# Optimization experiments

Hardware: AMD Instinct MI355X
Metric: run time of the kernel (lower is better)

## Reference

```python
import jax, jax.numpy as jnp
import numpy as np

DROPOUT_P = 0.1
DROPOUT_KEY = 42  # fixed key so the reference is deterministic


def setup_inputs() -> dict:
    key = jax.random.key(0)
    kx, kw = jax.random.split(key)
    B, N, D = 8, 2048, 1024
    x = jax.random.normal(kx, (B, N, D), dtype=jnp.float32)
    # xavier_uniform_ on [D, D]: U(-a, a), a = sqrt(6 / (D + D))
    a = np.sqrt(6.0 / (D + D)).astype(np.float32)
    weight = jax.random.uniform(kw, (D, D), dtype=jnp.float32, minval=-a, maxval=a)
    return {"x": x, "weight": weight}


def reference(x, weight):
    # bilinear scores: (x @ W) @ x^T  -> [B, N, N]
    scores = jnp.einsum("bnd,de,bme->bnm", x, weight, x)
    attn = jax.nn.softmax(scores, axis=-1)
    # dropout (train-mode, inverted scaling), deterministic key
    keep = jax.random.bernoulli(jax.random.key(DROPOUT_KEY), 1.0 - DROPOUT_P, attn.shape)
    attn = jnp.where(keep, attn / (1.0 - DROPOUT_P), 0.0)
    return jnp.einsum("bnm,bmd->bnd", attn, x)
```

## Files before the change

kernel.cpp:

```cpp
#include <hip/hip_runtime.h>
#include <hip/hip_fp16.h>
#include <stdint.h>

typedef __attribute__((ext_vector_type(8))) _Float16 f16x8;
typedef __attribute__((ext_vector_type(4))) float f32x4;
typedef __attribute__((ext_vector_type(8))) short s16x8;

#define MFMA_F16(a, b, c) __builtin_amdgcn_mfma_f32_16x16x32_f16((a), (b), (c), 0, 0, 0)
#define MFMA_BF16(a, b, c) __builtin_amdgcn_mfma_f32_16x16x32_bf16((a), (b), (c), 0, 0, 0)

__device__ __forceinline__ uint32_t pack_hi2(float f0, float f1, float& r0, float& r1) {
  uint32_t b0 = __float_as_uint(f0), b1 = __float_as_uint(f1);
  r0 = f0 - __uint_as_float(b0 & 0xFFFF0000u);
  r1 = f1 - __uint_as_float(b1 & 0xFFFF0000u);
  return (b1 & 0xFFFF0000u) | (b0 >> 16);
}
__device__ __forceinline__ uint32_t pack_lo2(float r0, float r1) {
  return (__float_as_uint(r1) & 0xFFFF0000u) | (__float_as_uint(r0) >> 16);
}
__device__ __forceinline__ uint32_t f16rn(float f) {
  return (uint32_t)__half_as_ushort(__float2half_rn(f));
}
__device__ __forceinline__ float f16tof(uint32_t h) {
  return __half2float(__ushort_as_half((unsigned short)h));
}

__device__ __forceinline__ uint2 threefry2x32_42(uint32_t x0, uint32_t x1) {
  const uint32_t ks0 = 0u, ks1 = 42u, ks2 = 0x1BD11BDAu ^ 42u;
  x0 += ks0; x1 += ks1;
#define TF_R(rot) { x0 += x1; x1 = ((x1 << rot) | (x1 >> (32 - rot))); x1 ^= x0; }
  TF_R(13) TF_R(15) TF_R(26) TF_R(6)   x0 += ks1; x1 += ks2 + 1u;
  TF_R(17) TF_R(29) TF_R(16) TF_R(24)  x0 += ks2; x1 += ks0 + 2u;
  TF_R(13) TF_R(15) TF_R(26) TF_R(6)   x0 += ks0; x1 += ks1 + 3u;
  TF_R(17) TF_R(29) TF_R(16) TF_R(24)  x0 += ks1; x1 += ks2 + 4u;
  TF_R(13) TF_R(15) TF_R(26) TF_R(6)   x0 += ks2; x1 += ks0 + 5u;
#undef TF_R
  return make_uint2(x0, x1);
}
__device__ __forceinline__ bool keep_bit(uint32_t j) {
  uint2 tf = threefry2x32_42(0u, j);
  uint32_t bits = tf.x ^ tf.y;
  return (__uint_as_float(0x3F800000u | (bits >> 9)) - 1.0f) < 0.9f;
}

__global__ __launch_bounds__(256) void w_splitT(const float* __restrict__ W,
    uint16_t* __restrict__ WhT, uint16_t* __restrict__ WlT) {
  __shared__ uint16_t th[64][72];
  __shared__ uint16_t tl[64][72];
  const int t = threadIdx.x;
  const int n0 = blockIdx.x * 64;
  const int k0 = blockIdx.y * 64;
  const int rr = t >> 2;
  const int cq = (t & 3) * 16;
  const float* src = W + (size_t)(k0 + rr) * 1024 + n0 + cq;
#pragma unroll
  for (int q = 0; q < 4; ++q) {
    float4 v = ((const float4*)src)[q];
    float e[4] = {v.x, v.y, v.z, v.w};
#pragma unroll
    for (int j = 0; j < 4; ++j) {
      uint32_t b = __float_as_uint(e[j]);
      float rem = e[j] - __uint_as_float(b & 0xFFFF0000u);
      th[cq + q * 4 + j][rr] = (uint16_t)(b >> 16);
      tl[cq + q * 4 + j][rr] = (uint16_t)(__float_as_uint(rem) >> 16);
    }
  }
  __syncthreads();
  size_t dst = (size_t)(n0 + rr) * 1024 + k0 + cq;
  *(uint4*)&WhT[dst] = *(const uint4*)&th[rr][cq];
  *(uint4*)&WhT[dst + 8] = *(const uint4*)&th[rr][cq + 8];
  *(uint4*)&WlT[dst] = *(const uint4*)&tl[rr][cq];
  *(uint4*)&WlT[dst + 8] = *(const uint4*)&tl[rr][cq + 8];
}

__global__ __launch_bounds__(256, 3) void bilin_gemm1w(
    const float* __restrict__ X, const uint16_t* __restrict__ WhT,
    const uint16_t* __restrict__ WlT, uint16_t* __restrict__ Yh,
    uint16_t* __restrict__ Yl) {
  __shared__ uint16_t sAh[128][40];
  __shared__ uint16_t sAl[128][40];
  __shared__ uint16_t sBh[128][40];
  __shared__ uint16_t sBl[128][40];

  const int t = threadIdx.x;
  const int lane = t & 63;
  const int wv = t >> 6;
  const int wm = wv >> 1, wn = wv & 1;
  const int lc = lane & 15, lg = lane >> 4;
  const int M0 = blockIdx.y * 128;
  const int N0 = blockIdx.x * 128;

  const f32x4 fzero = {0.f, 0.f, 0.f, 0.f};
  f32x4 acc[4][4];
#pragma unroll
  for (int i = 0; i < 4; ++i)
#pragma unroll
    for (int j = 0; j < 4; ++j) acc[i][j] = fzero;

  const int ar = t >> 1;
  const int ak = (t & 1) * 16;
  const int bc = t & 127;
  const int bq = t >> 7;

  const float* aptr = X + (size_t)(M0 + ar) * 1024 + ak;
  const uint16_t* whp = WhT + (size_t)(N0 + bc) * 1024 + bq * 16;
  const uint16_t* wlp = WlT + (size_t)(N0 + bc) * 1024 + bq * 16;

  for (int k0 = 0; k0 < 1024; k0 += 32) {
    {
      const float4* s = (const float4*)(aptr + k0);
#pragma unroll
      for (int q = 0; q < 2; ++q) {
        float4 v0 = s[q * 2 + 0];
        float4 v1 = s[q * 2 + 1];
        float r0, r1, r2, r3, r4, r5, r6, r7;
        uint32_t h0 = pack_hi2(v0.x, v0.y, r0, r1);
        uint32_t h1 = pack_hi2(v0.z, v0.w, r2, r3);
        uint32_t h2 = pack_hi2(v1.x, v1.y, r4, r5);
        uint32_t h3 = pack_hi2(v1.z, v1.w, r6, r7);
        uint32_t l0 = pack_lo2(r0, r1), l1 = pack_lo2(r2, r3);
        uint32_t l2 = pack_lo2(r4, r5), l3 = pack_lo2(r6, r7);
        *(uint4*)&sAh[ar][ak + q * 8] = make_uint4(h0, h1, h2, h3);
        *(uint4*)&sAl[ar][ak + q * 8] = make_uint4(l0, l1, l2, l3);
      }
    }
    {
      *(uint4*)&sBh[bc][bq * 16 + 0] = ((const uint4*)(whp + k0))[0];
      *(uint4*)&sBh[bc][bq * 16 + 8] = ((const uint4*)(whp + k0))[1];
      *(uint4*)&sBl[bc][bq * 16 + 0] = ((const uint4*)(wlp + k0))[0];
      *(uint4*)&sBl[bc][bq * 16 + 8] = ((const uint4*)(wlp + k0))[1];
    }
    __syncthreads();
    s16x8 ah[4], al[4];
#pragma unroll
    for (int mi = 0; mi < 4; ++mi) {
      ah[mi] = *(const s16x8*)&sAh[wm * 64 + mi * 16 + lc][lg * 8];
      al[mi] = *(const s16x8*)&sAl[wm * 64 + mi * 16 + lc][lg * 8];
    }
#pragma unroll
    for (int ni = 0; ni < 4; ++ni) {
      s16x8 bh = *(const s16x8*)&sBh[wn * 64 + ni * 16 + lc][lg * 8];
      s16x8 bl = *(const s16x8*)&sBl[wn * 64 + ni * 16 + lc][lg * 8];
#pragma unroll
      for (int mi = 0; mi < 4; ++mi) {
        acc[mi][ni] = MFMA_BF16(ah[mi], bh, acc[mi][ni]);
        acc[mi][ni] = MFMA_BF16(ah[mi], bl, acc[mi][ni]);
        acc[mi][ni] = MFMA_BF16(al[mi], bh, acc[mi][ni]);
      }
    }
    __syncthreads();
  }
#pragma unroll
  for (int mi = 0; mi < 4; ++mi)
#pragma unroll
    for (int ni = 0; ni < 4; ++ni)
#pragma unroll
      for (int r = 0; r < 4; ++r) {
        float y = acc[mi][ni][r];
        uint32_t hb = f16rn(y);
        uint32_t lb = f16rn(y - f16tof(hb));
        size_t idx = (size_t)(M0 + wm * 64 + mi * 16 + lg * 4 + r) * 1024 +
                     N0 + wn * 64 + ni * 16 + lc;
        Yh[idx] = (uint16_t)hb;
        Yl[idx] = (uint16_t)lb;
      }
}

__global__ __launch_bounds__(256) void pre_prep(const float* __restrict__ X,
    uint16_t* __restrict__ XhT, uint16_t* __restrict__ Xh) {
  __shared__ uint16_t tile[64][72];
  const int t = threadIdx.x;
  const int b = blockIdx.z;
  const int d0 = blockIdx.x * 64;
  const int k0 = blockIdx.y * 64;
  const int rr = t >> 2;
  const int cq = (t & 3) * 16;
  const float* src = X + (size_t)(b * 2048 + k0 + rr) * 1024 + d0 + cq;
  uint16_t hv[16];
#pragma unroll
  for (int q = 0; q < 4; ++q) {
    float4 v = ((const float4*)src)[q];
    hv[q * 4 + 0] = (uint16_t)f16rn(v.x);
    hv[q * 4 + 1] = (uint16_t)f16rn(v.y);
    hv[q * 4 + 2] = (uint16_t)f16rn(v.z);
    hv[q * 4 + 3] = (uint16_t)f16rn(v.w);
    tile[cq + q * 4 + 0][rr] = hv[q * 4 + 0];
    tile[cq + q * 4 + 1][rr] = hv[q * 4 + 1];
    tile[cq + q * 4 + 2][rr] = hv[q * 4 + 2];
    tile[cq + q * 4 + 3][rr] = hv[q * 4 + 3];
  }
  if (Xh) {
    size_t rowdst = (size_t)(b * 2048 + k0 + rr) * 1024 + d0 + cq;
    *(uint4*)&Xh[rowdst] = *(const uint4*)&hv[0];
    *(uint4*)&Xh[rowdst + 8] = *(const uint4*)&hv[8];
  }
  __syncthreads();
  uint16_t* dst = XhT + (size_t)(b * 1024 + d0 + rr) * 2048 + k0 + cq;
  *(uint4*)dst = *(const uint4*)&tile[rr][cq];
  *(uint4*)(dst + 8) = *(const uint4*)&tile[rr][cq + 8];
}

template <bool XH>
__global__ __launch_bounds__(256, 4) void bilin_score(
    const float* __restrict__ X, const uint16_t* __restrict__ Xh,
    const uint16_t* __restrict__ Yh, const uint16_t* __restrict__ Yl,
    uint16_t* __restrict__ Sp, float* __restrict__ Mt, float* __restrict__ Psum) {
  __shared__ uint16_t sAh[128][40];
  __shared__ uint16_t sAl[128][40];
  __shared__ uint16_t sBh[128][40];
  __shared__ float pm[2][128];
  __shared__ float psr[2][128];
  __shared__ float cm[128];

  const int t = threadIdx.x;
  const int lane = t & 63;
  const int wv = t >> 6;
  const int wm = wv >> 1, wn = wv & 1;
  const int lc = lane & 15, lg = lane >> 4;

  const int bid = blockIdx.x;
  const int b = bid & 7;
  const int tl = bid >> 3;
  const int M0 = (tl & 15) * 128;
  const int ktile = tl >> 4;
  const int N0 = ktile * 128;

  const float* Xb = X + (size_t)b * 2048 * 1024;

  const f32x4 fzero = {0.f, 0.f, 0.f, 0.f};
  f32x4 acc[4][4];
#pragma unroll
  for (int i = 0; i < 4; ++i)
#pragma unroll
    for (int j = 0; j < 4; ++j) acc[i][j] = fzero;

  const int ar = t >> 1;
  const int ak = (t & 1) * 16;

  const uint16_t* yhp = Yh + (size_t)(b * 2048 + M0 + ar) * 1024 + ak;
  const uint16_t* ylp = Yl + (size_t)(b * 2048 + M0 + ar) * 1024 + ak;
  const uint16_t* xhp = XH ? Xh + (size_t)(b * 2048 + N0 + ar) * 1024 + ak
                           : (const uint16_t*)nullptr;

  for (int k0 = 0; k0 < 1024; k0 += 32) {
    {
      *(uint4*)&sAh[ar][ak + 0] = ((const uint4*)(yhp + k0))[0];
      *(uint4*)&sAh[ar][ak + 8] = ((const uint4*)(yhp + k0))[1];
      *(uint4*)&sAl[ar][ak + 0] = ((const uint4*)(ylp + k0))[0];
      *(uint4*)&sAl[ar][ak + 8] = ((const uint4*)(ylp + k0))[1];
    }
    if constexpr (XH) {
      *(uint4*)&sBh[ar][ak + 0] = ((const uint4*)(xhp + k0))[0];
      *(uint4*)&sBh[ar][ak + 8] = ((const uint4*)(xhp + k0))[1];
    } else {
      const float4* bs = (const float4*)&Xb[(size_t)(N0 + ar) * 1024 + k0 + ak];
      uint32_t hp[8];
#pragma unroll
      for (int q = 0; q < 4; ++q) {
        float4 v = bs[q];
        hp[q * 2 + 0] = f16rn(v.x) | (f16rn(v.y) << 16);
        hp[q * 2 + 1] = f16rn(v.z) | (f16rn(v.w) << 16);
      }
      *(uint4*)&sBh[ar][ak + 0] = make_uint4(hp[0], hp[1], hp[2], hp[3]);
      *(uint4*)&sBh[ar][ak + 8] = make_uint4(hp[4], hp[5], hp[6], hp[7]);
    }
    __syncthreads();
    f16x8 ah[4], al[4];
#pragma unroll
    for (int mi = 0; mi < 4; ++mi) {
      ah[mi] = *(const f16x8*)&sAh[wm * 64 + mi * 16 + lc][lg * 8];
      al[mi] = *(const f16x8*)&sAl[wm * 64 + mi * 16 + lc][lg * 8];
    }
#pragma unroll
    for (int ni = 0; ni < 4; ++ni) {
      f16x8 bh = *(const f16x8*)&sBh[wn * 64 + ni * 16 + lc][lg * 8];
#pragma unroll
      for (int mi = 0; mi < 4; ++mi) {
        acc[mi][ni] = MFMA_F16(ah[mi], bh, acc[mi][ni]);
        acc[mi][ni] = MFMA_F16(al[mi], bh, acc[mi][ni]);
      }
    }
    __syncthreads();
  }

#pragma unroll
  for (int mi = 0; mi < 4; ++mi)
#pragma unroll
    for (int r = 0; r < 4; ++r) {
      float m = fmaxf(fmaxf(acc[mi][0][r], acc[mi][1][r]),
                      fmaxf(acc[mi][2][r], acc[mi][3][r]));
      m = fmaxf(m, __shfl_xor(m, 1, 64));
      m = fmaxf(m, __shfl_xor(m, 2, 64));
      m = fmaxf(m, __shfl_xor(m, 4, 64));
      m = fmaxf(m, __shfl_xor(m, 8, 64));
      if (lc == 0) pm[wn][wm * 64 + mi * 16 + lg * 4 + r] = m;
    }
  __syncthreads();
  if (t < 128) {
    float m = fmaxf(pm[0][t], pm[1][t]);
    cm[t] = m;
    Mt[((size_t)b * 16 + ktile) * 2048 + M0 + t] = m;
  }
  __syncthreads();

  uint16_t* Sb = Sp + (size_t)b * 2048 * 2048;
#pragma unroll
  for (int mi = 0; mi < 4; ++mi)
#pragma unroll
    for (int r = 0; r < 4; ++r) {
      const int rl = wm * 64 + mi * 16 + lg * 4 + r;
      const float m = cm[rl];
      const uint32_t jrow = (uint32_t)b * 4194304u + (uint32_t)(M0 + rl) * 2048u +
                            (uint32_t)(N0 + wn * 64) + (uint32_t)lc;
      float s = 0.0f;
#pragma unroll
      for (int ni = 0; ni < 4; ++ni) {
        float sv = acc[mi][ni][r] - m;
        s += __expf(sv);
        bool kp = keep_bit(jrow + ni * 16u);
        Sb[(size_t)(M0 + rl) * 2048 + N0 + wn * 64 + ni * 16 + lc] =
            kp ? (uint16_t)f16rn(sv) : (uint16_t)0xFC00u;
      }
      s += __shfl_xor(s, 1, 64);
      s += __shfl_xor(s, 2, 64);
      s += __shfl_xor(s, 4, 64);
      s += __shfl_xor(s, 8, 64);
      if (lc == 0) psr[wn][rl] = s;
    }
  __syncthreads();
  if (t < 128)
    Psum[((size_t)b * 16 + ktile) * 2048 + M0 + t] = psr[0][t] + psr[1][t];
}

__global__ __launch_bounds__(1024, 4) void bilin_pv(
    float* __restrict__ YO, const uint16_t* __restrict__ Sp,
    const float* __restrict__ Mt, const float* __restrict__ Psum,
    const uint16_t* __restrict__ XhT) {
  __shared__ __align__(16) uint16_t Pl[2][64][136];
  __shared__ float mts[64][17];
  __shared__ float mrowL[64], invL[64];

  const int t = threadIdx.x;
  const int lane = t & 63;
  const int wv = t >> 6;
  const int lc = lane & 15, lg = lane >> 4;

  const int b = blockIdx.x & 7;
  const int q0 = (blockIdx.x >> 3) * 64;

  const uint16_t* Sb = Sp + (size_t)b * 2048 * 2048;
  const uint16_t* Vb = XhT + (size_t)b * 1024 * 2048;

  const int row = t >> 4;
  const int sub = t & 15;

  {
    float mtv = Mt[((size_t)b * 16 + sub) * 2048 + q0 + row];
    float ps = Psum[((size_t)b * 16 + sub) * 2048 + q0 + row];
    mts[row][sub] = mtv;
    float m = mtv;
    m = fmaxf(m, __shfl_xor(m, 1, 64));
    m = fmaxf(m, __shfl_xor(m, 2, 64));
    m = fmaxf(m, __shfl_xor(m, 4, 64));
    m = fmaxf(m, __shfl_xor(m, 8, 64));
    float sc = ps * __expf(mtv - m);
    sc += __shfl_xor(sc, 1, 64);
    sc += __shfl_xor(sc, 2, 64);
    sc += __shfl_xor(sc, 4, 64);
    sc += __shfl_xor(sc, 8, 64);
    if (sub == 0) { mrowL[row] = m; invL[row] = 1.0f / (sc * 0.9f); }
  }
  __syncthreads();

  const f32x4 fzero = {0.f, 0.f, 0.f, 0.f};
  f32x4 acc[4][4];
#pragma unroll
  for (int i = 0; i < 4; ++i)
#pragma unroll
    for (int j = 0; j < 4; ++j) acc[i][j] = fzero;

  const int d0 = wv * 64;
  const float mrL = mrowL[row];

  auto stage = [&](uint4 su, int kt, int buf) {
    const float mdel = mts[row][kt] - mrL;
    float p0 = __expf(f16tof(su.x & 0xFFFFu) + mdel);
    float p1 = __expf(f16tof(su.x >> 16) + mdel);
    float p2 = __expf(f16tof(su.y & 0xFFFFu) + mdel);
    float p3 = __expf(f16tof(su.y >> 16) + mdel);
    float p4 = __expf(f16tof(su.z & 0xFFFFu) + mdel);
    float p5 = __expf(f16tof(su.z >> 16) + mdel);
    float p6 = __expf(f16tof(su.w & 0xFFFFu) + mdel);
    float p7 = __expf(f16tof(su.w >> 16) + mdel);
    uint32_t w0 = f16rn(p0) | (f16rn(p1) << 16);
    uint32_t w1 = f16rn(p2) | (f16rn(p3) << 16);
    uint32_t w2 = f16rn(p4) | (f16rn(p5) << 16);
    uint32_t w3 = f16rn(p6) | (f16rn(p7) << 16);
    *(uint4*)&Pl[buf][row][sub * 8] = make_uint4(w0, w1, w2, w3);
  };

  uint4 su = *(const uint4*)&Sb[(size_t)(q0 + row) * 2048 + 0 * 128 + sub * 8];
  stage(su, 0, 0);
  __syncthreads();

  for (int kt = 0; kt < 16; ++kt) {
    const int cb = kt & 1;
    uint4 sun;
    if (kt < 15)
      sun = *(const uint4*)&Sb[(size_t)(q0 + row) * 2048 + (kt + 1) * 128 + sub * 8];
#pragma unroll
    for (int kst = 0; kst < 4; ++kst) {
      f16x8 a0 = *(const f16x8*)&Pl[cb][0 * 16 + lc][kst * 32 + lg * 8];
      f16x8 a1 = *(const f16x8*)&Pl[cb][1 * 16 + lc][kst * 32 + lg * 8];
      f16x8 a2 = *(const f16x8*)&Pl[cb][2 * 16 + lc][kst * 32 + lg * 8];
      f16x8 a3 = *(const f16x8*)&Pl[cb][3 * 16 + lc][kst * 32 + lg * 8];
#pragma unroll
      for (int nc = 0; nc < 4; ++nc) {
        f16x8 v = *(const f16x8*)&Vb[(size_t)(d0 + nc * 16 + lc) * 2048 +
                                     kt * 128 + kst * 32 + lg * 8];
        acc[0][nc] = MFMA_F16(a0, v, acc[0][nc]);
        acc[1][nc] = MFMA_F16(a1, v, acc[1][nc]);
        acc[2][nc] = MFMA_F16(a2, v, acc[2][nc]);
        acc[3][nc] = MFMA_F16(a3, v, acc[3][nc]);
      }
    }
    if (kt < 15) stage(sun, kt + 1, cb ^ 1);
    __syncthreads();
  }

  float* outb = YO + (size_t)b * 2048 * 1024;
#pragma unroll
  for (int fr = 0; fr < 4; ++fr)
#pragma unroll
    for (int r = 0; r < 4; ++r) {
      const int rl = fr * 16 + lg * 4 + r;
      const float inv = invL[rl];
#pragma unroll
      for (int nc = 0; nc < 4; ++nc)
        outb[(size_t)(q0 + rl) * 1024 + d0 + nc * 16 + lc] = acc[fr][nc][r] * inv;
    }
}

__global__ __launch_bounds__(256, 3) void bilin_gemm1(
    const float* __restrict__ X, const float* __restrict__ W,
    uint32_t* __restrict__ Ypk) {
  __shared__ uint16_t sAh[128][40];
  __shared__ uint16_t sAl[128][40];
  __shared__ uint16_t sBh[128][40];
  __shared__ uint16_t sBl[128][40];

  const int t = threadIdx.x;
  const int lane = t & 63;
  const int wv = t >> 6;
  const int wm = wv >> 1, wn = wv & 1;
  const int lc = lane & 15, lg = lane >> 4;
  const int M0 = blockIdx.y * 128;
  const int N0 = blockIdx.x * 128;

  const f32x4 fzero = {0.f, 0.f, 0.f, 0.f};
  f32x4 acc[4][4];
#pragma unroll
  for (int i = 0; i < 4; ++i)
#pragma unroll
    for (int j = 0; j < 4; ++j) acc[i][j] = fzero;

  const int ar = t >> 1;
  const int ak = (t & 1) * 16;
  const int bc = t & 127;
  const int bq = t >> 7;

  const float* aptr = X + (size_t)(M0 + ar) * 1024 + ak;
  const float* bptr = W + (size_t)bq * 16 * 1024 + N0 + bc;

  for (int k0 = 0; k0 < 1024; k0 += 32) {
    {
      const float4* s = (const float4*)(aptr + k0);
#pragma unroll
      for (int q = 0; q < 2; ++q) {
        float4 v0 = s[q * 2 + 0];
        float4 v1 = s[q * 2 + 1];
        float r0, r1, r2, r3, r4, r5, r6, r7;
        uint32_t h0 = pack_hi2(v0.x, v0.y, r0, r1);
        uint32_t h1 = pack_hi2(v0.z, v0.w, r2, r3);
        uint32_t h2 = pack_hi2(v1.x, v1.y, r4, r5);
        uint32_t h3 = pack_hi2(v1.z, v1.w, r6, r7);
        uint32_t l0 = pack_lo2(r0, r1), l1 = pack_lo2(r2, r3);
        uint32_t l2 = pack_lo2(r4, r5), l3 = pack_lo2(r6, r7);
        *(uint4*)&sAh[ar][ak + q * 8] = make_uint4(h0, h1, h2, h3);
        *(uint4*)&sAl[ar][ak + q * 8] = make_uint4(l0, l1, l2, l3);
      }
    }
    {
      float v[16];
#pragma unroll
      for (int i = 0; i < 16; ++i) v[i] = bptr[(size_t)(k0 + i) * 1024];
      float r[16];
      uint32_t h[8], lo[8];
#pragma unroll
      for (int i = 0; i < 8; ++i) h[i] = pack_hi2(v[2 * i], v[2 * i + 1], r[2 * i], r[2 * i + 1]);
#pragma unroll
      for (int i = 0; i < 8; ++i) lo[i] = pack_lo2(r[2 * i], r[2 * i + 1]);
      *(uint4*)&sBh[bc][bq * 16 + 0] = make_uint4(h[0], h[1], h[2], h[3]);
      *(uint4*)&sBh[bc][bq * 16 + 8] = make_uint4(h[4], h[5], h[6], h[7]);
      *(uint4*)&sBl[bc][bq * 16 + 0] = make_uint4(lo[0], lo[1], lo[2], lo[3]);
      *(uint4*)&sBl[bc][bq * 16 + 8] = make_uint4(lo[4], lo[5], lo[6], lo[7]);
    }
    __syncthreads();
    s16x8 ah[4], al[4];
#pragma unroll
    for (int mi = 0; mi < 4; ++mi) {
      ah[mi] = *(const s16x8*)&sAh[wm * 64 + mi * 16 + lc][lg * 8];
      al[mi] = *(const s16x8*)&sAl[wm * 64 + mi * 16 + lc][lg * 8];
    }
#pragma unroll
    for (int ni = 0; ni < 4; ++ni) {
      s16x8 bh = *(const s16x8*)&sBh[wn * 64 + ni * 16 + lc][lg * 8];
      s16x8 bl = *(const s16x8*)&sBl[wn * 64 + ni * 16 + lc][lg * 8];
#pragma unroll
      for (int mi = 0; mi < 4; ++mi) {
        acc[mi][ni] = MFMA_BF16(ah[mi], bh, acc[mi][ni]);
        acc[mi][ni] = MFMA_BF16(ah[mi], bl, acc[mi][ni]);
        acc[mi][ni] = MFMA_BF16(al[mi], bh, acc[mi][ni]);
      }
    }
    __syncthreads();
  }
#pragma unroll
  for (int mi = 0; mi < 4; ++mi)
#pragma unroll
    for (int ni = 0; ni < 4; ++ni)
#pragma unroll
      for (int r = 0; r < 4; ++r) {
        float y = acc[mi][ni][r];
        uint32_t hb = f16rn(y);
        uint32_t lb = f16rn(y - f16tof(hb));
        int row = M0 + wm * 64 + mi * 16 + lg * 4 + r;
        int col = N0 + wn * 64 + ni * 16 + lc;
        Ypk[(size_t)row * 1024 + col] = (hb << 16) | lb;
      }
}

__global__ __launch_bounds__(512, 4) void bilin_flash2f(
    const float* __restrict__ X, float* __restrict__ YO) {
  __shared__ __align__(16) uint16_t kbuf[2][2][128][40];
  __shared__ __align__(16) uint16_t qbuf[2][2][32][40];
  __shared__ __align__(16) uint16_t Pl[32][136];
  __shared__ float red[8][16];
  __shared__ float mrow[32], lrow[32], frow[32];
  uint16_t* vbase = &kbuf[0][0][0][0];

  const int t = threadIdx.x;
  const int lane = t & 63;
  const int wv = t >> 6;
  const int wr = wv >> 2, wc = wv & 3;
  const int lc = lane & 15, lg = lane >> 4;
  const int b = blockIdx.x & 7;
  const int q0 = (blockIdx.x >> 3) * 32;

  const float* Xb = X + (size_t)b * 2048 * 1024;
  const uint32_t* Ypk = (const uint32_t*)YO;

  if (t < 32) { mrow[t] = -1e30f; lrow[t] = 0.0f; }

  const f32x4 fzero = {0.f, 0.f, 0.f, 0.f};
  f32x4 acc_pv[16];
#pragma unroll
  for (int c = 0; c < 16; ++c) acc_pv[c] = fzero;

  const int myrow = wr * 16 + lg * 4;
  const int qsr = t >> 3;
  const int qsc = (t & 7) * 4;
  const int ksk = t >> 2;
  const int ksd = (t & 3) * 8;
  const int vkp = t & 63;
  const int vdg = t >> 6;

  for (int kb = 0; kb < 16; ++kb) {
    const int kbase = kb * 128;
    __syncthreads();

    f32x4 acc_s0 = fzero, acc_s1 = fzero;
    uint4 qld;
    float4 kf0, kf1;

    auto load_q = [&](int dd) {
      if (t < 256) qld = *(const uint4*)&Ypk[(size_t)(b * 2048 + q0 + qsr) * 1024 + dd + qsc];
    };
    auto write_q = [&](int nb) {
      if (t < 256) {
        uint32_t hh0 = (qld.x >> 16) | (qld.y & 0xFFFF0000u);
        uint32_t hh1 = (qld.z >> 16) | (qld.w & 0xFFFF0000u);
        uint32_t ll0 = (qld.x & 0xFFFFu) | (qld.y << 16);
        uint32_t ll1 = (qld.z & 0xFFFFu) | (qld.w << 16);
        *(uint2*)&qbuf[nb][0][qsr][qsc] = make_uint2(hh0, hh1);
        *(uint2*)&qbuf[nb][1][qsr][qsc] = make_uint2(ll0, ll1);
      }
    };
    auto load_k = [&](int dd) {
      const float* s = &Xb[(size_t)(kbase + ksk) * 1024 + dd + ksd];
      kf0 = ((const float4*)s)[0];
      kf1 = ((const float4*)s)[1];
    };
    auto write_k = [&](int nb) {
      float e[8] = {kf0.x, kf0.y, kf0.z, kf0.w, kf1.x, kf1.y, kf1.z, kf1.w};
      uint32_t h[8], l[8];
#pragma unroll
      for (int j = 0; j < 8; ++j) {
        h[j] = f16rn(e[j]);
        l[j] = f16rn(e[j] - f16tof(h[j]));
      }
      *(uint4*)&kbuf[nb][0][ksk][ksd] =
          make_uint4(h[0] | (h[1] << 16), h[2] | (h[3] << 16), h[4] | (h[5] << 16), h[6] | (h[7] << 16));
      *(uint4*)&kbuf[nb][1][ksk][ksd] =
          make_uint4(l[0] | (l[1] << 16), l[2] | (l[3] << 16), l[4] | (l[5] << 16), l[6] | (l[7] << 16));
    };

    load_q(0); load_k(0);
    write_q(0); write_k(0);
    __syncthreads();
#pragma unroll 2
    for (int dc = 0; dc < 32; ++dc) {
      const int cb = dc & 1;
      if (dc < 31) { load_q((dc + 1) * 32); load_k((dc + 1) * 32); }
      f16x8 ah = *(const f16x8*)&qbuf[cb][0][wr * 16 + lc][lg * 8];
      f16x8 al = *(const f16x8*)&qbuf[cb][1][wr * 16 + lc][lg * 8];
      {
        f16x8 bh = *(const f16x8*)&kbuf[cb][0][wc * 32 + lc][lg * 8];
        f16x8 bl = *(const f16x8*)&kbuf[cb][1][wc * 32 + lc][lg * 8];
        acc_s0 = MFMA_F16(ah, bh, acc_s0);
        acc_s0 = MFMA_F16(ah, bl, acc_s0);
        acc_s0 = MFMA_F16(al, bh, acc_s0);
      }
      {
        f16x8 bh = *(const f16x8*)&kbuf[cb][0][wc * 32 + 16 + lc][lg * 8];
        f16x8 bl = *(const f16x8*)&kbuf[cb][1][wc * 32 + 16 + lc][lg * 8];
        acc_s1 = MFMA_F16(ah, bh, acc_s1);
        acc_s1 = MFMA_F16(ah, bl, acc_s1);
        acc_s1 = MFMA_F16(al, bh, acc_s1);
      }
      if (dc < 31) { write_q(cb ^ 1); write_k(cb ^ 1); __syncthreads(); }
    }

#pragma unroll
    for (int r = 0; r < 4; ++r) {
      float m = fmaxf(acc_s0[r], acc_s1[r]);
      m = fmaxf(m, __shfl_xor(m, 1, 64));
      m = fmaxf(m, __shfl_xor(m, 2, 64));
      m = fmaxf(m, __shfl_xor(m, 4, 64));
      m = fmaxf(m, __shfl_xor(m, 8, 64));
      if (lc == 0) red[wv][lg * 4 + r] = m;
    }
    __syncthreads();
    if (t < 32) {
      int wrr = t >> 4, rr = t & 15;
      float mk = fmaxf(fmaxf(red[wrr * 4 + 0][rr], red[wrr * 4 + 1][rr]),
                       fmaxf(red[wrr * 4 + 2][rr], red[wrr * 4 + 3][rr]));
      float mo = mrow[t], mn = fmaxf(mo, mk);
      mrow[t] = mn;
      frow[t] = __expf(mo - mn);
    }
    __syncthreads();
#pragma unroll
    for (int r = 0; r < 4; ++r) {
      const int row = myrow + r;
      const float mn = mrow[row];
      float p0 = __expf(acc_s0[r] - mn);
      float p1 = __expf(acc_s1[r] - mn);
      float s = p0 + p1;
      s += __shfl_xor(s, 1, 64);
      s += __shfl_xor(s, 2, 64);
      s += __shfl_xor(s, 4, 64);
      s += __shfl_xor(s, 8, 64);
      if (lc == 0) red[wv][lg * 4 + r] = s;
      uint32_t jr = (uint32_t)b * 4194304u + (uint32_t)(q0 + row) * 2048u +
                    (uint32_t)(kbase + wc * 32 + lc);
      bool k0 = keep_bit(jr);
      bool k1 = keep_bit(jr + 16u);
      Pl[row][wc * 32 + lc] = k0 ? (uint16_t)f16rn(p0) : (uint16_t)0;
      Pl[row][wc * 32 + 16 + lc] = k1 ? (uint16_t)f16rn(p1) : (uint16_t)0;
    }
    __syncthreads();
    if (t < 32) {
      int wrr = t >> 4, rr = t & 15;
      lrow[t] = lrow[t] * frow[t] + (red[wrr * 4 + 0][rr] + red[wrr * 4 + 1][rr] +
                                     red[wrr * 4 + 2][rr] + red[wrr * 4 + 3][rr]);
    }

    {
      float fr[4];
#pragma unroll
      for (int r = 0; r < 4; ++r) fr[r] = frow[myrow + r];
#pragma unroll
      for (int c = 0; c < 16; ++c)
#pragma unroll
        for (int r = 0; r < 4; ++r) acc_pv[c][r] *= fr[r];
    }
    f16x8 ap0 = *(const f16x8*)&Pl[wr * 16 + lc][0 * 32 + lg * 8];
    f16x8 ap1 = *(const f16x8*)&Pl[wr * 16 + lc][1 * 32 + lg * 8];
    f16x8 ap2 = *(const f16x8*)&Pl[wr * 16 + lc][2 * 32 + lg * 8];
    f16x8 ap3 = *(const f16x8*)&Pl[wr * 16 + lc][3 * 32 + lg * 8];

    float4 vf0, vf1, vf2, vf3;
    auto load_v = [&](int c) {
      const float* s0 = &Xb[(size_t)(kbase + vkp * 2) * 1024 + c * 64 + vdg * 8];
      vf0 = ((const float4*)s0)[0];
      vf1 = ((const float4*)s0)[1];
      vf2 = ((const float4*)(s0 + 1024))[0];
      vf3 = ((const float4*)(s0 + 1024))[1];
    };
    auto write_v = [&](int nb) {
      uint16_t* vt = vbase + nb * (64 * 136);
      float a[8] = {vf0.x, vf0.y, vf0.z, vf0.w, vf1.x, vf1.y, vf1.z, vf1.w};
      float b2[8] = {vf2.x, vf2.y, vf2.z, vf2.w, vf3.x, vf3.y, vf3.z, vf3.w};
#pragma unroll
      for (int j = 0; j < 8; ++j)
        *(uint32_t*)&vt[(vdg * 8 + j) * 136 + vkp * 2] = f16rn(a[j]) | (f16rn(b2[j]) << 16);
    };

    load_v(0); write_v(0);
    __syncthreads();
#pragma unroll
    for (int c = 0; c < 16; ++c) {
      const int cb = c & 1;
      if (c < 15) load_v(c + 1);
      const uint16_t* vt = vbase + cb * (64 * 136);
      f16x8 bf0 = *(const f16x8*)&vt[(wc * 16 + lc) * 136 + 0 * 32 + lg * 8];
      f16x8 bf1 = *(const f16x8*)&vt[(wc * 16 + lc) * 136 + 1 * 32 + lg * 8];
      f16x8 bf2 = *(const f16x8*)&vt[(wc * 16 + lc) * 136 + 2 * 32 + lg * 8];
      f16x8 bf3 = *(const f16x8*)&vt[(wc * 16 + lc) * 136 + 3 * 32 + lg * 8];
      acc_pv[c] = MFMA_F16(ap0, bf0, acc_pv[c]);
      acc_pv[c] = MFMA_F16(ap1, bf1, acc_pv[c]);
      acc_pv[c] = MFMA_F16(ap2, bf2, acc_pv[c]);
      acc_pv[c] = MFMA_F16(ap3, bf3, acc_pv[c]);
      if (c < 15) { write_v(cb ^ 1); __syncthreads(); }
    }
  }

  __syncthreads();
  float inv[4];
#pragma unroll
  for (int r = 0; r < 4; ++r) inv[r] = 1.0f / (lrow[myrow + r] * 0.9f);
  float* outb = YO + (size_t)b * 2048 * 1024;
#pragma unroll
  for (int c = 0; c < 16; ++c)
#pragma unroll
    for (int r = 0; r < 4; ++r)
      outb[(size_t)(q0 + myrow + r) * 1024 + c * 64 + wc * 16 + lc] = acc_pv[c][r] * inv[r];
}

extern "C" void kernel_launch(void* const* d_in, const int* in_sizes, int n_in,
                              void* d_out, int out_size, void* d_ws, size_t ws_size,
                              hipStream_t stream) {
  (void)in_sizes; (void)n_in; (void)out_size;
  const float* X = (const float*)d_in[0];
  const float* W = (const float*)d_in[1];
  const bool mid = ws_size >= 104857600ULL;
  const bool big = ws_size >= 140509184ULL;

  if (mid) {
    uint16_t* XhT = (uint16_t*)d_ws;
    uint16_t* Sp = (uint16_t*)((char*)d_ws + 33554432);
    uint16_t* WhT = (uint16_t*)((char*)d_ws + 100663296);
    uint16_t* WlT = (uint16_t*)((char*)d_ws + 100663296 + 2097152);
    float* Mt = (float*)((char*)d_ws + 100663296);
    float* Psum = (float*)((char*)d_ws + 100663296 + 1048576);
    uint16_t* Xh = big ? (uint16_t*)((char*)d_ws + 106954752) : nullptr;
    uint16_t* Yh = (uint16_t*)d_out;
    uint16_t* Yl = Yh + 16777216;

    w_splitT<<<dim3(16, 16), 256, 0, stream>>>(W, WhT, WlT);
    bilin_gemm1w<<<dim3(8, 128), 256, 0, stream>>>(X, WhT, WlT, Yh, Yl);
    pre_prep<<<dim3(16, 32, 8), 256, 0, stream>>>(X, XhT, Xh);
    if (big)
      bilin_score<true><<<2048, 256, 0, stream>>>(X, Xh, Yh, Yl, Sp, Mt, Psum);
    else
      bilin_score<false><<<2048, 256, 0, stream>>>(X, nullptr, Yh, Yl, Sp, Mt, Psum);
    bilin_pv<<<256, 1024, 0, stream>>>((float*)d_out, Sp, Mt, Psum, XhT);
  } else {
    bilin_gemm1<<<dim3(8, 128), 256, 0, stream>>>(X, W, (uint32_t*)d_out);
    bilin_flash2f<<<512, 512, 0, stream>>>(X, (float*)d_out);
  }
}
```

Baseline: 575.4 us.

## Prefetch next K-tile into registers while computing current tile in GEMM kernels

Both the X·W GEMM and the scores GEMM now issue global loads for the next K-slice into registers before running the MFMA work on the current shared-memory tile. The staged values are written to LDS after a barrier. This is meant to hide global memory latency behind the matrix-core work. It raises register pressure, which could lower occupancy, and keeps two barriers per iteration.

New measurement: 549.2 us. 4.5% less time.

```diff
diff --git a/kernel.cpp b/kernel.cpp
--- a/kernel.cpp
+++ b/kernel.cpp
@@ -106,31 +106,44 @@
   const uint16_t* whp = WhT + (size_t)(N0 + bc) * 1024 + bq * 16;
   const uint16_t* wlp = WlT + (size_t)(N0 + bc) * 1024 + bq * 16;
 
-  for (int k0 = 0; k0 < 1024; k0 += 32) {
-    {
-      const float4* s = (const float4*)(aptr + k0);
-#pragma unroll
-      for (int q = 0; q < 2; ++q) {
-        float4 v0 = s[q * 2 + 0];
-        float4 v1 = s[q * 2 + 1];
-        float r0, r1, r2, r3, r4, r5, r6, r7;
-        uint32_t h0 = pack_hi2(v0.x, v0.y, r0, r1);
-        uint32_t h1 = pack_hi2(v0.z, v0.w, r2, r3);
-        uint32_t h2 = pack_hi2(v1.x, v1.y, r4, r5);
-        uint32_t h3 = pack_hi2(v1.z, v1.w, r6, r7);
-        uint32_t l0 = pack_lo2(r0, r1), l1 = pack_lo2(r2, r3);
-        uint32_t l2 = pack_lo2(r4, r5), l3 = pack_lo2(r6, r7);
-        *(uint4*)&sAh[ar][ak + q * 8] = make_uint4(h0, h1, h2, h3);
-        *(uint4*)&sAl[ar][ak + q * 8] = make_uint4(l0, l1, l2, l3);
-      }
-    }
-    {
-      *(uint4*)&sBh[bc][bq * 16 + 0] = ((const uint4*)(whp + k0))[0];
-      *(uint4*)&sBh[bc][bq * 16 + 8] = ((const uint4*)(whp + k0))[1];
-      *(uint4*)&sBl[bc][bq * 16 + 0] = ((const uint4*)(wlp + k0))[0];
-      *(uint4*)&sBl[bc][bq * 16 + 8] = ((const uint4*)(wlp + k0))[1];
-    }
-    __syncthreads();
+  float4 rA0, rA1, rA2, rA3;
+  uint4 rBh0, rBh1, rBl0, rBl1;
+
+  auto loadT = [&](int k0) {
+    const float4* s = (const float4*)(aptr + k0);
+    rA0 = s[0]; rA1 = s[1]; rA2 = s[2]; rA3 = s[3];
+    rBh0 = ((const uint4*)(whp + k0))[0];
+    rBh1 = ((const uint4*)(whp + k0))[1];
+    rBl0 = ((const uint4*)(wlp + k0))[0];
+    rBl1 = ((const uint4*)(wlp + k0))[1];
+  };
+  auto writeT = [&]() {
+    float r0, r1, r2, r3, r4, r5, r6, r7, r8, r9, rA, rB, rC, rD, rE, rF;
+    uint32_t h0 = pack_hi2(rA0.x, rA0.y, r0, r1);
+    uint32_t h1 = pack_hi2(rA0.z, rA0.w, r2, r3);
+    uint32_t h2 = pack_hi2(rA1.x, rA1.y, r4, r5);
+    uint32_t h3 = pack_hi2(rA1.z, rA1.w, r6, r7);
+    uint32_t h4 = pack_hi2(rA2.x, rA2.y, r8, r9);
+    uint32_t h5 = pack_hi2(rA2.z, rA2.w, rA, rB);
+    uint32_t h6 = pack_hi2(rA3.x, rA3.y, rC, rD);
+    uint32_t h7 = pack_hi2(rA3.z, rA3.w, rE, rF);
+    *(uint4*)&sAh[ar][ak + 0] = make_uint4(h0, h1, h2, h3);
+    *(uint4*)&sAh[ar][ak + 8] = make_uint4(h4, h5, h6, h7);
+    *(uint4*)&sAl[ar][ak + 0] =
+        make_uint4(pack_lo2(r0, r1), pack_lo2(r2, r3), pack_lo2(r4, r5), pack_lo2(r6, r7));
+    *(uint4*)&sAl[ar][ak + 8] =
+        make_uint4(pack_lo2(r8, r9), pack_lo2(rA, rB), pack_lo2(rC, rD), pack_lo2(rE, rF));
+    *(uint4*)&sBh[bc][bq * 16 + 0] = rBh0;
+    *(uint4*)&sBh[bc][bq * 16 + 8] = rBh1;
+    *(uint4*)&sBl[bc][bq * 16 + 0] = rBl0;
+    *(uint4*)&sBl[bc][bq * 16 + 8] = rBl1;
+  };
+
+  loadT(0);
+  writeT();
+  __syncthreads();
+  for (int it = 0; it < 32; ++it) {
+    if (it < 31) loadT((it + 1) * 32);
     s16x8 ah[4], al[4];
 #pragma unroll
     for (int mi = 0; mi < 4; ++mi) {
@@ -148,7 +161,11 @@
         acc[mi][ni] = MFMA_BF16(al[mi], bh, acc[mi][ni]);
       }
     }
-    __syncthreads();
+    if (it < 31) {
+      __syncthreads();
+      writeT();
+      __syncthreads();
+    }
   }
 #pragma unroll
   for (int mi = 0; mi < 4; ++mi)
@@ -242,29 +259,50 @@
   const uint16_t* xhp = XH ? Xh + (size_t)(b * 2048 + N0 + ar) * 1024 + ak
                            : (const uint16_t*)nullptr;
 
-  for (int k0 = 0; k0 < 1024; k0 += 32) {
-    {
-      *(uint4*)&sAh[ar][ak + 0] = ((const uint4*)(yhp + k0))[0];
-      *(uint4*)&sAh[ar][ak + 8] = ((const uint4*)(yhp + k0))[1];
-      *(uint4*)&sAl[ar][ak + 0] = ((const uint4*)(ylp + k0))[0];
-      *(uint4*)&sAl[ar][ak + 8] = ((const uint4*)(ylp + k0))[1];
-    }
+  uint4 rAh0, rAh1, rAl0, rAl1;
+  uint4 rB0, rB1;
+  float4 rBf0, rBf1, rBf2, rBf3;
+
+  auto loadT = [&](int k0) {
+    rAh0 = ((const uint4*)(yhp + k0))[0];
+    rAh1 = ((const uint4*)(yhp + k0))[1];
+    rAl0 = ((const uint4*)(ylp + k0))[0];
+    rAl1 = ((const uint4*)(ylp + k0))[1];
     if constexpr (XH) {
-      *(uint4*)&sBh[ar][ak + 0] = ((const uint4*)(xhp + k0))[0];
-      *(uint4*)&sBh[ar][ak + 8] = ((const uint4*)(xhp + k0))[1];
+      rB0 = ((const uint4*)(xhp + k0))[0];
+      rB1 = ((const uint4*)(xhp + k0))[1];
     } else {
       const float4* bs = (const float4*)&Xb[(size_t)(N0 + ar) * 1024 + k0 + ak];
-      uint32_t hp[8];
-#pragma unroll
-      for (int q = 0; q < 4; ++q) {
-        float4 v = bs[q];
-        hp[q * 2 + 0] = f16rn(v.x) | (f16rn(v.y) << 16);
-        hp[q * 2 + 1] = f16rn(v.z) | (f16rn(v.w) << 16);
-      }
-      *(uint4*)&sBh[ar][ak + 0] = make_uint4(hp[0], hp[1], hp[2], hp[3]);
-      *(uint4*)&sBh[ar][ak + 8] = make_uint4(hp[4], hp[5], hp[6], hp[7]);
-    }
-    __syncthreads();
+      rBf0 = bs[0]; rBf1 = bs[1]; rBf2 = bs[2]; rBf3 = bs[3];
+    }
+  };
+  auto writeT = [&]() {
+    *(uint4*)&sAh[ar][ak + 0] = rAh0;
+    *(uint4*)&sAh[ar][ak + 8] = rAh1;
+    *(uint4*)&sAl[ar][ak + 0] = rAl0;
+    *(uint4*)&sAl[ar][ak + 8] = rAl1;
+    if constexpr (XH) {
+      *(uint4*)&sBh[ar][ak + 0] = rB0;
+      *(uint4*)&sBh[ar][ak + 8] = rB1;
+    } else {
+      uint32_t h0 = f16rn(rBf0.x) | (f16rn(rBf0.y) << 16);
+      uint32_t h1 = f16rn(rBf0.z) | (f16rn(rBf0.w) << 16);
+      uint32_t h2 = f16rn(rBf1.x) | (f16rn(rBf1.y) << 16);
+      uint32_t h3 = f16rn(rBf1.z) | (f16rn(rBf1.w) << 16);
+      uint32_t h4 = f16rn(rBf2.x) | (f16rn(rBf2.y) << 16);
+      uint32_t h5 = f16rn(rBf2.z) | (f16rn(rBf2.w) << 16);
+      uint32_t h6 = f16rn(rBf3.x) | (f16rn(rBf3.y) << 16);
+      uint32_t h7 = f16rn(rBf3.z) | (f16rn(rBf3.w) << 16);
+      *(uint4*)&sBh[ar][ak + 0] = make_uint4(h0, h1, h2, h3);
+      *(uint4*)&sBh[ar][ak + 8] = make_uint4(h4, h5, h6, h7);
+    }
+  };
+
+  loadT(0);
+  writeT();
+  __syncthreads();
+  for (int it = 0; it < 32; ++it) {
+    if (it < 31) loadT((it + 1) * 32);
     f16x8 ah[4], al[4];
 #pragma unroll
     for (int mi = 0; mi < 4; ++mi) {
@@ -280,7 +318,11 @@
         acc[mi][ni] = MFMA_F16(al[mi], bh, acc[mi][ni]);
       }
     }
-    __syncthreads();
+    if (it < 31) {
+      __syncthreads();
+      writeT();
+      __syncthreads();
+    }
   }
 
 #pragma unroll
```
